# Kernel tuning notes

Hardware: AMD Instinct MI355X
Metric: run time of the kernel (lower is better)

Reference implementation:

```python
import jax, jax.numpy as jnp
import numpy as np

N_NODES = 100000
N_EDGES = 3200000
C_IN = 128
C_OUT = 128
K = 4

def setup_inputs() -> dict:
    key = jax.random.key(0)
    k1, k2, k3, k4, k5 = jax.random.split(key, 5)
    x = jax.random.normal(k1, (N_NODES, C_IN), dtype=jnp.float32)
    # per-edge Laplacian values, scaled so the Chebyshev recurrence stays bounded
    lap = jax.random.normal(k2, (N_EDGES,), dtype=jnp.float32) * 0.05
    stdv = 1.0 / np.sqrt(C_IN * K)
    weight = jax.random.uniform(k3, (K, C_IN, C_OUT), dtype=jnp.float32, minval=-stdv, maxval=stdv)
    bias = jax.random.uniform(k4, (C_OUT,), dtype=jnp.float32, minval=-stdv, maxval=stdv)
    edge_index = jax.random.randint(k5, (2, N_EDGES), 0, N_NODES, dtype=jnp.int64)
    return {"x": x, "lap": lap, "weight": weight, "bias": bias,
            "edge_index": edge_index, "num_nodes": N_NODES}

def _spmm(edge_index, lap, num_nodes, x):
    # y[row] += lap_e * x[col] for each edge e = (row, col)
    row, col = edge_index[0], edge_index[1]
    msgs = lap[:, None] * x[col]            # [E, C]
    return jax.ops.segment_sum(msgs, row, num_segments=num_nodes)

def reference(x, lap, weight, bias, edge_index, num_nodes):
    K_ = weight.shape[0]
    Tx_0 = x                                 # T_0(L) x = x
    out = Tx_0 @ weight[0]
    if K_ > 1:
        Tx_1 = _spmm(edge_index, lap, num_nodes, x)   # T_1(L) x = L x
        out = out + Tx_1 @ weight[1]
    for k in range(2, K_):
        Tx_2 = 2.0 * _spmm(edge_index, lap, num_nodes, Tx_1) - Tx_0
        out = out + Tx_2 @ weight[k]
        Tx_0, Tx_1 = Tx_1, Tx_2
    return out + bias
```

## Files before the change

kernel.cpp:

```cpp
#include <hip/hip_runtime.h>

#define N_NODES 100000
#define N_EDGES 3200000
#define ROWS_PAD 100032
#define N_BUCKETS 782
#define BUCKET_SHIFT 7

typedef __attribute__((ext_vector_type(8))) short bf16x8;
typedef __attribute__((ext_vector_type(4))) float f32x4;
typedef __attribute__((ext_vector_type(2))) float f32x2;

__device__ __forceinline__ unsigned short f2bf(float f) {
    unsigned u = __float_as_uint(f);
    unsigned r = (u + 0x7fffu + ((u >> 16) & 1u)) >> 16;
    return (unsigned short)r;
}
__device__ __forceinline__ float bflo(unsigned u) { return __uint_as_float(u << 16); }
__device__ __forceinline__ float bfhi(unsigned u) { return __uint_as_float(u & 0xffff0000u); }

__global__ void __launch_bounds__(256) k_convert_x(const float* __restrict__ x,
                                                   unsigned* __restrict__ xf8) {
    const int QTOT = ROWS_PAD * 32;
    for (int q = blockIdx.x * 256 + threadIdx.x; q < QTOT; q += 1024 * 256) {
        int r = q >> 5;
        f32x4 f = {0.f, 0.f, 0.f, 0.f};
        if (r < N_NODES) f = *(const f32x4*)(x + 4 * (size_t)q);
        int pk = __builtin_amdgcn_cvt_pk_fp8_f32(f.x, f.y, 0, false);
        pk = __builtin_amdgcn_cvt_pk_fp8_f32(f.z, f.w, pk, true);
        xf8[q] = (unsigned)pk;
    }
}

__global__ void k_convert_w(const float* __restrict__ w, unsigned short* __restrict__ wt) {
    int i = blockIdx.x * 256 + threadIdx.x;
    int m = i >> 14, rem = i & 16383, k = rem >> 7, c = rem & 127;
    wt[(m << 14) + (c << 7) + k] = f2bf(w[i]);
}

__global__ void __launch_bounds__(256) k_bhist(const int* __restrict__ ei, int* __restrict__ bcnt) {
    __shared__ int h[N_BUCKETS];
    for (int i = threadIdx.x; i < N_BUCKETS; i += 256) h[i] = 0;
    __syncthreads();
    int base = blockIdx.x * 8192;
#pragma unroll
    for (int i = 0; i < 32; ++i) {
        int e = base + threadIdx.x + i * 256;
        if (e < N_EDGES) atomicAdd(&h[ei[e] >> BUCKET_SHIFT], 1);
    }
    __syncthreads();
    for (int i = threadIdx.x; i < N_BUCKETS; i += 256)
        if (h[i]) atomicAdd(&bcnt[i], h[i]);
}

__global__ void __launch_bounds__(1024) k_bscan(const int* __restrict__ bcnt,
                                                int* __restrict__ bbase,
                                                int* __restrict__ bcursor,
                                                int* __restrict__ rowstart,
                                                int2* __restrict__ ep) {
    __shared__ int s[1024];
    int t = threadIdx.x;
    int v = (t < N_BUCKETS) ? bcnt[t] : 0;
    s[t] = v;
    __syncthreads();
    for (int off = 1; off < 1024; off <<= 1) {
        int tv = (t >= off) ? s[t - off] : 0;
        __syncthreads();
        s[t] += tv;
        __syncthreads();
    }
    if (t < N_BUCKETS) {
        int ex = s[t] - v;
        bbase[t] = ex;
        bcursor[t] = ex;
    }
    if (t == 0) {
        bbase[N_BUCKETS] = N_EDGES;
        rowstart[N_NODES] = N_EDGES;
    }
    if (t < 64) ep[N_EDGES + t] = make_int2(0, 0);
}

__global__ void __launch_bounds__(1024) k_bin(const int* __restrict__ ei,
                                              const float* __restrict__ lap,
                                              int* __restrict__ bcursor,
                                              uint2* __restrict__ ep_tmp) {
    __shared__ int h[N_BUCKETS];
    __shared__ int runbase[N_BUCKETS];
    for (int i = threadIdx.x; i < N_BUCKETS; i += 1024) h[i] = 0;
    __syncthreads();
    int base = blockIdx.x * 16384;
#pragma unroll
    for (int i = 0; i < 16; ++i) {
        int e = base + threadIdx.x + i * 1024;
        if (e < N_EDGES) atomicAdd(&h[ei[e] >> BUCKET_SHIFT], 1);
    }
    __syncthreads();
    for (int i = threadIdx.x; i < N_BUCKETS; i += 1024) {
        int c = h[i];
        runbase[i] = c ? atomicAdd(&bcursor[i], c) : 0;
        h[i] = 0;
    }
    __syncthreads();
#pragma unroll
    for (int i = 0; i < 16; ++i) {
        int e = base + threadIdx.x + i * 1024;
        if (e < N_EDGES) {
            int row = ei[e], col = ei[N_EDGES + e];
            int b = row >> BUCKET_SHIFT;
            int p = runbase[b] + atomicAdd(&h[b], 1);
            ep_tmp[p] = make_uint2(((unsigned)(row & 127) << 17) | (unsigned)col,
                                   __float_as_uint(lap[e]));
        }
    }
}

#define ST_CAP 5120
__global__ void __launch_bounds__(256) k_rsort(const uint2* __restrict__ ep_tmp,
                                               const int* __restrict__ bbase,
                                               int* __restrict__ rowstart,
                                               int2* __restrict__ ep) {
    __shared__ uint2 st[ST_CAP];
    __shared__ int h[128];
    __shared__ int lcur[128];
    int b = blockIdx.x;
    int base = bbase[b], end = bbase[b + 1];
    int n = end - base;
    if (n > ST_CAP) n = ST_CAP;
    for (int i = threadIdx.x; i < n; i += 256) st[i] = ep_tmp[base + i];
    if (threadIdx.x < 128) h[threadIdx.x] = 0;
    __syncthreads();
    for (int i = threadIdx.x; i < n; i += 256) atomicAdd(&h[st[i].x >> 17], 1);
    __syncthreads();
    int t = threadIdx.x;
    int v = (t < 128) ? h[t] : 0;
    for (int off = 1; off < 128; off <<= 1) {
        int tv = (t < 128 && t >= off) ? h[t - off] : 0;
        __syncthreads();
        if (t < 128) h[t] += tv;
        __syncthreads();
    }
    if (t < 128) {
        int ex = h[t] - v;
        int r = (b << BUCKET_SHIFT) + t;
        if (r < N_NODES) rowstart[r] = base + ex;
        lcur[t] = base + ex;
    }
    __syncthreads();
    for (int i = threadIdx.x; i < n; i += 256) {
        uint2 s = st[i];
        int r = s.x >> 17;
        int p = atomicAdd(&lcur[r], 1);
        ep[p] = make_int2((int)(s.x & 0x1FFFFu), (int)s.y);
    }
}

__global__ void __launch_bounds__(256) k_spmm8(
    const unsigned char* __restrict__ xs, const void* __restrict__ z, int zmode,
    unsigned* __restrict__ y8, uint2* __restrict__ yb,
    const int* __restrict__ rowstart, const int2* __restrict__ ep, float a, float b)
{
    int wv = threadIdx.x >> 6, lane = threadIdx.x & 63;
    int r = blockIdx.x * 4 + wv;
    if (r >= N_NODES) return;
    int q = lane >> 4, s = lane & 15;
    unsigned vs8 = (unsigned)s * 8u;
    int bp0 = (q) * 4, bp1 = (4 + q) * 4, bp2 = (8 + q) * 4, bp3 = (12 + q) * 4;
    float acc0 = 0.f, acc1 = 0.f, acc2 = 0.f, acc3 = 0.f;
    float acc4 = 0.f, acc5 = 0.f, acc6 = 0.f, acc7 = 0.f;
    int e0 = rowstart[r], e1 = rowstart[r + 1];
    int cnt = e1 - e0;
    if (cnt > 0) {
        int niter = (cnt + 15) >> 4;
        int nfull = cnt >> 4;
        const char* epb = (const char*)ep;

#define LOADEP(p, itv) do {                                              \
        int _idx = e0 + (itv) * 16 + s;                                  \
        int2 _t = *(const int2*)(epb + (unsigned)_idx * 8u);             \
        if ((itv) >= nfull) {                   \
            bool _v = _idx < e1;                                         \
            _t.x = _v ? _t.x : 0;          \
            _t.y = _v ? _t.y : 0;         \
        }                                                                \
        p = _t;                                                          \
    } while (0)
#define BPERM(cc, ll, p) do {                                            \
        cc[0] = __builtin_amdgcn_ds_bpermute(bp0, (p).x);                \
        cc[1] = __builtin_amdgcn_ds_bpermute(bp1, (p).x);                \
        cc[2] = __builtin_amdgcn_ds_bpermute(bp2, (p).x);                \
        cc[3] = __builtin_amdgcn_ds_bpermute(bp3, (p).x);                \
        ll[0] = __builtin_amdgcn_ds_bpermute(bp0, (p).y);                \
        ll[1] = __builtin_amdgcn_ds_bpermute(bp1, (p).y);                \
        ll[2] = __builtin_amdgcn_ds_bpermute(bp2, (p).y);                \
        ll[3] = __builtin_amdgcn_ds_bpermute(bp3, (p).y);                \
    } while (0)
#define GATHER(G, cc) do {                                               \
        _Pragma("unroll")                                                \
        for (int _u = 0; _u < 4; ++_u)                                   \
            G[_u] = *(const uint2*)(xs + ((((unsigned)cc[_u]) << 7) + vs8)); \
    } while (0)
#define CONSUME(G, ll) do {                                              \
        _Pragma("unroll")                                                \
        for (int _u = 0; _u < 4; ++_u) {                                 \
            float _l = __int_as_float(ll[_u]);                           \
            f32x2 _f0 = __builtin_amdgcn_cvt_pk_f32_fp8((int)G[_u].x, false); \
            f32x2 _f1 = __builtin_amdgcn_cvt_pk_f32_fp8((int)G[_u].x, true);  \
            f32x2 _f2 = __builtin_amdgcn_cvt_pk_f32_fp8((int)G[_u].y, false); \
            f32x2 _f3 = __builtin_amdgcn_cvt_pk_f32_fp8((int)G[_u].y, true);  \
            acc0 += _l * _f0.x; acc1 += _l * _f0.y;                      \
            acc2 += _l * _f1.x; acc3 += _l * _f1.y;                      \
            acc4 += _l * _f2.x; acc5 += _l * _f2.y;                      \
            acc6 += _l * _f3.x; acc7 += _l * _f3.y;                      \
        }                                                                \
    } while (0)

        int2 pA, pB;
        int cA[4], cB[4], lA[4], lB[4];
        uint2 GA[4], GB[4];

        LOADEP(pA, 0);
        BPERM(cA, lA, pA);
        GATHER(GA, cA);
        int it = 0;
        while (it + 2 <= niter) {
            LOADEP(pB, it + 1);
            BPERM(cB, lB, pB);
            GATHER(GB, cB);
            CONSUME(GA, lA);
            if (it + 2 < niter) {
                LOADEP(pA, it + 2);
                BPERM(cA, lA, pA);
                GATHER(GA, cA);
            }
            CONSUME(GB, lB);
            it += 2;
        }
        if (it < niter) CONSUME(GA, lA);
#undef LOADEP
#undef BPERM
#undef GATHER
#undef CONSUME
    }
    acc0 += __shfl(acc0, lane ^ 16, 64); acc1 += __shfl(acc1, lane ^ 16, 64);
    acc2 += __shfl(acc2, lane ^ 16, 64); acc3 += __shfl(acc3, lane ^ 16, 64);
    acc4 += __shfl(acc4, lane ^ 16, 64); acc5 += __shfl(acc5, lane ^ 16, 64);
    acc6 += __shfl(acc6, lane ^ 16, 64); acc7 += __shfl(acc7, lane ^ 16, 64);
    acc0 += __shfl(acc0, lane ^ 32, 64); acc1 += __shfl(acc1, lane ^ 32, 64);
    acc2 += __shfl(acc2, lane ^ 32, 64); acc3 += __shfl(acc3, lane ^ 32, 64);
    acc4 += __shfl(acc4, lane ^ 32, 64); acc5 += __shfl(acc5, lane ^ 32, 64);
    acc6 += __shfl(acc6, lane ^ 32, 64); acc7 += __shfl(acc7, lane ^ 32, 64);
    if (q == 0) {
        float o0 = a * acc0, o1 = a * acc1, o2 = a * acc2, o3 = a * acc3;
        float o4 = a * acc4, o5 = a * acc5, o6 = a * acc6, o7 = a * acc7;
        if (zmode == 1) {
            uint4 zg = *((const uint4*)z + (size_t)r * 16 + s);
            o0 += b * bflo(zg.x); o1 += b * bfhi(zg.x);
            o2 += b * bflo(zg.y); o3 += b * bfhi(zg.y);
            o4 += b * bflo(zg.z); o5 += b * bfhi(zg.z);
            o6 += b * bflo(zg.w); o7 += b * bfhi(zg.w);
        } else if (zmode == 3) {
            const f32x4* zp = (const f32x4*)z + (size_t)r * 32 + s * 2;
            f32x4 z0 = zp[0], z1 = zp[1];
            o0 += b * z0.x; o1 += b * z0.y; o2 += b * z0.z; o3 += b * z0.w;
            o4 += b * z1.x; o5 += b * z1.y; o6 += b * z1.z; o7 += b * z1.w;
        }
        uint4 ob;
        ob.x = (unsigned)f2bf(o0) | ((unsigned)f2bf(o1) << 16);
        ob.y = (unsigned)f2bf(o2) | ((unsigned)f2bf(o3) << 16);
        ob.z = (unsigned)f2bf(o4) | ((unsigned)f2bf(o5) << 16);
        ob.w = (unsigned)f2bf(o6) | ((unsigned)f2bf(o7) << 16);
        *((uint4*)yb + (size_t)r * 16 + s) = ob;
        if (y8) {
            int pk0 = __builtin_amdgcn_cvt_pk_fp8_f32(o0, o1, 0, false);
            pk0 = __builtin_amdgcn_cvt_pk_fp8_f32(o2, o3, pk0, true);
            int pk1 = __builtin_amdgcn_cvt_pk_fp8_f32(o4, o5, 0, false);
            pk1 = __builtin_amdgcn_cvt_pk_fp8_f32(o6, o7, pk1, true);
            *((uint2*)y8 + (size_t)r * 16 + s) = make_uint2((unsigned)pk0, (unsigned)pk1);
        }
    }
}

__device__ __forceinline__ void load_afrags(const void* A, int fmt, int row, int quad,
                                            bf16x8* frag) {
    if (fmt == 0) {
        const short* p = (const short*)A + (size_t)row * 128 + quad * 8;
#pragma unroll
        for (int kk = 0; kk < 4; ++kk) frag[kk] = *(const bf16x8*)(p + kk * 32);
    } else {
        const float* p = (const float*)A + (size_t)row * 128 + quad * 8;
#pragma unroll
        for (int kk = 0; kk < 4; ++kk) {
            f32x4 u = *(const f32x4*)(p + kk * 32);
            f32x4 v = *(const f32x4*)(p + kk * 32 + 4);
            bf16x8 fr;
            fr[0] = (short)f2bf(u.x); fr[1] = (short)f2bf(u.y);
            fr[2] = (short)f2bf(u.z); fr[3] = (short)f2bf(u.w);
            fr[4] = (short)f2bf(v.x); fr[5] = (short)f2bf(v.y);
            fr[6] = (short)f2bf(v.z); fr[7] = (short)f2bf(v.w);
            frag[kk] = fr;
        }
    }
}

__global__ void __launch_bounds__(256) k_gemm2(
    const void* __restrict__ A0, int fmt0, const unsigned short* __restrict__ WT0,
    const void* __restrict__ A1, int fmt1, const unsigned short* __restrict__ WT1,
    float* __restrict__ out, const float* __restrict__ bias, int mode)
{
    int wv = threadIdx.x >> 6, lane = threadIdx.x & 63;
    int m = lane & 15, quad = lane >> 4;
    int r0 = blockIdx.x * 64 + wv * 16;
    int row = r0 + m;
    int row0 = (fmt0 == 1 && row >= N_NODES) ? (N_NODES - 1) : row;
    int row1 = (fmt1 == 1 && row >= N_NODES) ? (N_NODES - 1) : row;
    bf16x8 a0[4], a1[4];
    load_afrags(A0, fmt0, row0, quad, a0);
    load_afrags(A1, fmt1, row1, quad, a1);
#pragma unroll
    for (int ct = 0; ct < 8; ++ct) {
        int c0 = ct * 16;
        const short* Bp0 = (const short*)WT0 + (c0 + m) * 128 + quad * 8;
        const short* Bp1 = (const short*)WT1 + (c0 + m) * 128 + quad * 8;
        f32x4 acc0 = {0.f, 0.f, 0.f, 0.f};
        f32x4 acc1 = {0.f, 0.f, 0.f, 0.f};
#pragma unroll
        for (int kk = 0; kk < 4; ++kk) {
            bf16x8 b0 = *(const bf16x8*)(Bp0 + kk * 32);
            bf16x8 b1 = *(const bf16x8*)(Bp1 + kk * 32);
            acc0 = __builtin_amdgcn_mfma_f32_16x16x32_bf16(a0[kk], b0, acc0, 0, 0, 0);
            acc1 = __builtin_amdgcn_mfma_f32_16x16x32_bf16(a1[kk], b1, acc1, 0, 0, 0);
        }
        int c = c0 + m;
#pragma unroll
        for (int i = 0; i < 4; ++i) {
            int r = r0 + quad * 4 + i;
            if (r < N_NODES) {
                float* o = out + (size_t)r * 128 + c;
                float v = acc0[i] + acc1[i];
                if (mode == 0) *o = v;
                else           *o = *o + v + bias[c];
            }
        }
    }
}

extern "C" void kernel_launch(void* const* d_in, const int* in_sizes, int n_in,
                              void* d_out, int out_size, void* d_ws, size_t ws_size,
                              hipStream_t stream) {
    const float* x    = (const float*)d_in[0];
    const float* lap  = (const float*)d_in[1];
    const float* w    = (const float*)d_in[2];
    const float* bias = (const float*)d_in[3];
    const int*   ei   = (const int*)d_in[4];
    float* out = (float*)d_out;

    char* ws = (char*)d_ws;
    const size_t SZ_BF = (size_t)ROWS_PAD * 128 * 2;
    const size_t SZ_F8 = (size_t)ROWS_PAD * 128;
    const size_t SZ_EP = SZ_BF + 1024;
    int2* ep            = (int2*)(ws);
    unsigned char* xf8  = (unsigned char*)(ws + SZ_EP);
    unsigned char* t1_8 = (unsigned char*)(ws + SZ_EP + SZ_F8);
    unsigned char* t3_b = (unsigned char*)(ws + SZ_EP);
    unsigned char* t1_b = (unsigned char*)(ws + SZ_EP + SZ_BF);
    unsigned char* t2_8 = (unsigned char*)(ws + SZ_EP + 2 * SZ_BF);
    unsigned char* t2_b = (unsigned char*)(ws + SZ_EP + 2 * SZ_BF + SZ_F8);
    uint2* ep_tmp       = (uint2*)(ws + SZ_EP + 2 * SZ_BF);
    char* p = ws + SZ_EP + 3 * SZ_BF + SZ_F8;
    int* rowstart = (int*)p; p += 400128;
    int* bcnt     = (int*)p; p += 3200;
    int* bbase    = (int*)p; p += 3200;
    int* bcursor  = (int*)p; p += 3200;
    unsigned short* wt = (unsigned short*)p;

    hipMemsetAsync(bcnt, 0, N_BUCKETS * sizeof(int), stream);
    k_convert_x<<<1024, 256, 0, stream>>>(x, (unsigned*)xf8);
    k_convert_w<<<256, 256, 0, stream>>>(w, wt);
    k_bhist<<<(N_EDGES + 8191) / 8192, 256, 0, stream>>>(ei, bcnt);
    k_bscan<<<1, 1024, 0, stream>>>(bcnt, bbase, bcursor, rowstart, ep);
    k_bin<<<(N_EDGES + 16383) / 16384, 1024, 0, stream>>>(ei, lap, bcursor, ep_tmp);
    k_rsort<<<N_BUCKETS, 256, 0, stream>>>(ep_tmp, bbase, rowstart, ep);

    k_spmm8<<<ROWS_PAD / 4, 256, 0, stream>>>(xf8, nullptr, 0,
        (unsigned*)t1_8, (uint2*)t1_b, rowstart, ep, 1.f, 0.f);
    k_gemm2<<<ROWS_PAD / 64, 256, 0, stream>>>(x, 1, wt, t1_b, 0, wt + 16384, out, bias, 0);
    k_spmm8<<<ROWS_PAD / 4, 256, 0, stream>>>(t1_8, x, 3,
        (unsigned*)t2_8, (uint2*)t2_b, rowstart, ep, 2.f, -1.f);
    k_spmm8<<<ROWS_PAD / 4, 256, 0, stream>>>(t2_8, t1_b, 1,
        nullptr, (uint2*)t3_b, rowstart, ep, 2.f, -1.f);
    k_gemm2<<<ROWS_PAD / 64, 256, 0, stream>>>(t2_b, 0, wt + 2 * 16384, t3_b, 0, wt + 3 * 16384, out, bias, 1);
}
```

Measured before the change: 575.7 us.

## Fuse two GEMM passes into one four-term GEMM with LDS-staged coalesced stores

```diff
diff --git a/kernel.cpp b/kernel.cpp
--- a/kernel.cpp
+++ b/kernel.cpp
@@ -302,45 +302,56 @@
     }
 }
 
-__global__ void __launch_bounds__(256) k_gemm2(
-    const void* __restrict__ A0, int fmt0, const unsigned short* __restrict__ WT0,
-    const void* __restrict__ A1, int fmt1, const unsigned short* __restrict__ WT1,
-    float* __restrict__ out, const float* __restrict__ bias, int mode)
+__global__ void __launch_bounds__(256) k_gemm4(
+    const float* __restrict__ x,
+    const unsigned short* __restrict__ t1,
+    const unsigned short* __restrict__ t2,
+    const unsigned short* __restrict__ t3,
+    const unsigned short* __restrict__ wt,
+    float* __restrict__ out, const float* __restrict__ bias)
 {
+    __shared__ float cbuf[4][16 * 132];
     int wv = threadIdx.x >> 6, lane = threadIdx.x & 63;
     int m = lane & 15, quad = lane >> 4;
     int r0 = blockIdx.x * 64 + wv * 16;
     int row = r0 + m;
-    int row0 = (fmt0 == 1 && row >= N_NODES) ? (N_NODES - 1) : row;
-    int row1 = (fmt1 == 1 && row >= N_NODES) ? (N_NODES - 1) : row;
-    bf16x8 a0[4], a1[4];
-    load_afrags(A0, fmt0, row0, quad, a0);
-    load_afrags(A1, fmt1, row1, quad, a1);
+    int rowc = (row >= N_NODES) ? (N_NODES - 1) : row;
+    bf16x8 a0[4], a1[4], a2[4], a3[4];
+    load_afrags(x,  1, rowc, quad, a0);
+    load_afrags(t1, 0, row,  quad, a1);
+    load_afrags(t2, 0, row,  quad, a2);
+    load_afrags(t3, 0, row,  quad, a3);
+    float* cw = &cbuf[wv][0];
 #pragma unroll
     for (int ct = 0; ct < 8; ++ct) {
         int c0 = ct * 16;
-        const short* Bp0 = (const short*)WT0 + (c0 + m) * 128 + quad * 8;
-        const short* Bp1 = (const short*)WT1 + (c0 + m) * 128 + quad * 8;
-        f32x4 acc0 = {0.f, 0.f, 0.f, 0.f};
-        f32x4 acc1 = {0.f, 0.f, 0.f, 0.f};
+        const short* B0 = (const short*)wt + (c0 + m) * 128 + quad * 8;
+        f32x4 accA = {0.f, 0.f, 0.f, 0.f};
+        f32x4 accB = {0.f, 0.f, 0.f, 0.f};
 #pragma unroll
         for (int kk = 0; kk < 4; ++kk) {
-            bf16x8 b0 = *(const bf16x8*)(Bp0 + kk * 32);
-            bf16x8 b1 = *(const bf16x8*)(Bp1 + kk * 32);
-            acc0 = __builtin_amdgcn_mfma_f32_16x16x32_bf16(a0[kk], b0, acc0, 0, 0, 0);
-            acc1 = __builtin_amdgcn_mfma_f32_16x16x32_bf16(a1[kk], b1, acc1, 0, 0, 0);
-        }
-        int c = c0 + m;
-#pragma unroll
-        for (int i = 0; i < 4; ++i) {
-            int r = r0 + quad * 4 + i;
-            if (r < N_NODES) {
-                float* o = out + (size_t)r * 128 + c;
-                float v = acc0[i] + acc1[i];
-                if (mode == 0) *o = v;
-                else           *o = *o + v + bias[c];
-            }
-        }
+            bf16x8 b0 = *(const bf16x8*)(B0 + kk * 32);
+            bf16x8 b1 = *(const bf16x8*)(B0 + 16384 + kk * 32);
+            bf16x8 b2 = *(const bf16x8*)(B0 + 32768 + kk * 32);
+            bf16x8 b3 = *(const bf16x8*)(B0 + 49152 + kk * 32);
+            accA = __builtin_amdgcn_mfma_f32_16x16x32_bf16(a0[kk], b0, accA, 0, 0, 0);
+            accB = __builtin_amdgcn_mfma_f32_16x16x32_bf16(a1[kk], b1, accB, 0, 0, 0);
+            accA = __builtin_amdgcn_mfma_f32_16x16x32_bf16(a2[kk], b2, accA, 0, 0, 0);
+            accB = __builtin_amdgcn_mfma_f32_16x16x32_bf16(a3[kk], b3, accB, 0, 0, 0);
+        }
+#pragma unroll
+        for (int i = 0; i < 4; ++i)
+            cw[(quad * 4 + i) * 132 + c0 + m] = accA[i] + accB[i];
+    }
+    int er = lane >> 2, ec = (lane & 3) * 32;
+    int gr = r0 + er;
+#pragma unroll
+    for (int j = 0; j < 8; ++j) {
+        f32x4 v = *(f32x4*)(cw + er * 132 + ec + j * 4);
+        f32x4 bb = *(const f32x4*)(bias + ec + j * 4);
+        v.x += bb.x; v.y += bb.y; v.z += bb.z; v.w += bb.w;
+        if (gr < N_NODES)
+            *(f32x4*)(out + (size_t)gr * 128 + ec + j * 4) = v;
     }
 }
 
@@ -383,10 +394,10 @@
 
     k_spmm8<<<ROWS_PAD / 4, 256, 0, stream>>>(xf8, nullptr, 0,
         (unsigned*)t1_8, (uint2*)t1_b, rowstart, ep, 1.f, 0.f);
-    k_gemm2<<<ROWS_PAD / 64, 256, 0, stream>>>(x, 1, wt, t1_b, 0, wt + 16384, out, bias, 0);
     k_spmm8<<<ROWS_PAD / 4, 256, 0, stream>>>(t1_8, x, 3,
         (unsigned*)t2_8, (uint2*)t2_b, rowstart, ep, 2.f, -1.f);
     k_spmm8<<<ROWS_PAD / 4, 256, 0, stream>>>(t2_8, t1_b, 1,
         nullptr, (uint2*)t3_b, rowstart, ep, 2.f, -1.f);
-    k_gemm2<<<ROWS_PAD / 64, 256, 0, stream>>>(t2_b, 0, wt + 2 * 16384, t3_b, 0, wt + 3 * 16384, out, bias, 1);
-}
+    k_gemm4<<<ROWS_PAD / 64, 256, 0, stream>>>(x, (const unsigned short*)t1_b,
+        (const unsigned short*)t2_b, (const unsigned short*)t3_b, wt, out, bias);
+}
```

Result: no change. 579.4 us (+0.6%).
